# Performance work log

Hardware: AMD Instinct MI355X
Metric: run time of the kernel (lower is better)

The kernel has to match this reference:

```python
import jax, jax.numpy as jnp
import numpy as np

B, S, DM = 2, 2048, 1024
H, KH, HD = 16, 4, 64  # query heads, kv heads, head_dim
N_REP = H // KH


def rotate_half(u):
    d = u.shape[-1] // 2
    return jnp.concatenate([-u[..., d:], u[..., :d]], axis=-1)


def setup_inputs() -> dict:
    key = jax.random.key(0)
    ks = jax.random.split(key, 7)
    x = jax.random.normal(ks[0], (B, S, DM), dtype=jnp.float32)
    # RoPE tables (real rotary angles for realism)
    inv_freq = 1.0 / (10000.0 ** (jnp.arange(0, HD, 2, dtype=jnp.float32) / HD))
    t = jnp.arange(S, dtype=jnp.float32)
    freqs = jnp.outer(t, inv_freq)                      # [S, HD/2]
    emb = jnp.concatenate([freqs, freqs], axis=-1)      # [S, HD]
    cos, sin = jnp.cos(emb), jnp.sin(emb)
    sc = 0.02
    wq = jax.random.normal(ks[1], (DM, H * HD), dtype=jnp.float32) * sc
    wk = jax.random.normal(ks[2], (DM, KH * HD), dtype=jnp.float32) * sc
    wv = jax.random.normal(ks[3], (DM, KH * HD), dtype=jnp.float32) * sc
    wo = jax.random.normal(ks[4], (H * HD, DM), dtype=jnp.float32) * sc
    return {"x": x, "cos": cos, "sin": sin, "wq": wq, "wk": wk, "wv": wv, "wo": wo}


def reference(x, cos, sin, wq, wk, wv, wo):
    b, s, _ = x.shape
    # QKV projections (no bias)
    q = (x @ wq).reshape(b, s, H, HD)   # [b,s,H,HD]
    k = (x @ wk).reshape(b, s, KH, HD)  # [b,s,KH,HD]
    v = (x @ wv).reshape(b, s, KH, HD)
    # RoPE, broadcast cos/sin over the head axis
    c = cos[None, :s, None, :]
    sn = sin[None, :s, None, :]
    q = q * c + rotate_half(q) * sn
    k = k * c + rotate_half(k) * sn
    # GQA: repeat kv heads (repeat_interleave along head axis)
    k = jnp.repeat(k, N_REP, axis=2)  # [b,s,H,HD]
    v = jnp.repeat(v, N_REP, axis=2)
    # causal attention, full score matrix (non-flash path)
    scores = jnp.einsum("bqhd,bkhd->bhqk", q, k) / jnp.sqrt(jnp.float32(HD))
    causal = jnp.tril(jnp.ones((s, s), dtype=bool))
    scores = jnp.where(causal[None, None], scores, jnp.float32(-jnp.inf))
    attn = jax.nn.softmax(scores, axis=-1)
    out = jnp.einsum("bhqk,bkhd->bqhd", attn, v).reshape(b, s, H * HD)
    return out @ wo
```

## Files before the change

kernel.cpp:

```cpp
#include <hip/hip_runtime.h>
#include <hip/hip_bf16.h>

#define BATCH 2
#define SLEN  2048
#define DM    1024
#define NH    16
#define NKH   4
#define HD    64
#define NCH   4
#define PSTRIDE (BATCH * SLEN * NH * HD)
#define LSTRIDE (BATCH * SLEN * NH)

typedef __attribute__((ext_vector_type(8))) short short8;
typedef __attribute__((ext_vector_type(4))) float f32x4;

static __device__ __forceinline__ short f2bf(float x) {
    unsigned u = __float_as_uint(x);
    u += 0x7fffu + ((u >> 16) & 1u);
    return (short)(u >> 16);
}

static __device__ __forceinline__ void ldg_lds16(const short* g, short* l) {
    __builtin_amdgcn_global_load_lds(
        (const __attribute__((address_space(1))) unsigned int*)(const void*)g,
        (__attribute__((address_space(3))) unsigned int*)(void*)l,
        16, 0, 0);
}

#define QSCALE 0.1803368801f

__global__ void cvt_bf16(const float* __restrict__ X, short* __restrict__ Xb, int total8)
{
    const int i = blockIdx.x * blockDim.x + threadIdx.x;
    if (i >= total8) return;
    const float4 v0 = ((const float4*)X)[i * 2];
    const float4 v1 = ((const float4*)X)[i * 2 + 1];
    __align__(16) short o[8];
    o[0] = f2bf(v0.x); o[1] = f2bf(v0.y); o[2] = f2bf(v0.z); o[3] = f2bf(v0.w);
    o[4] = f2bf(v1.x); o[5] = f2bf(v1.y); o[6] = f2bf(v1.z); o[7] = f2bf(v1.w);
    ((int4*)Xb)[i] = *(const int4*)o;
}

__global__ __launch_bounds__(256) void wtrans_all(
    const float* __restrict__ wq, const float* __restrict__ wk,
    const float* __restrict__ wv, const float* __restrict__ wo,
    short* __restrict__ T)
{
    const int by = blockIdx.y;
    const float* W; int Nc, rowoff, ntile;
    if (by < 16)      { W = wq; Nc = 1024; rowoff = 0;    ntile = by; }
    else if (by < 20) { W = wk; Nc = 256;  rowoff = 1024; ntile = by - 16; }
    else if (by < 24) { W = wv; Nc = 256;  rowoff = 1280; ntile = by - 20; }
    else              { W = wo; Nc = 1024; rowoff = 1536; ntile = by - 24; }
    const int kt = blockIdx.x * 64;
    const int nt = ntile * 64;
    const int t  = threadIdx.x;
    __shared__ float tile[64][65];

#pragma unroll
    for (int i = 0; i < 4; ++i) {
        const int r = (t >> 4) + i * 16;
        const int c = (t & 15) * 4;
        const float4 v = *(const float4*)(W + (size_t)(kt + r) * Nc + nt + c);
        tile[r][c + 0] = v.x; tile[r][c + 1] = v.y;
        tile[r][c + 2] = v.z; tile[r][c + 3] = v.w;
    }
    __syncthreads();
#pragma unroll
    for (int i = 0; i < 2; ++i) {
        const int rr = (t >> 3) + i * 32;
        const int cc = (t & 7) * 8;
        __align__(16) short o[8];
#pragma unroll
        for (int j = 0; j < 8; ++j) o[j] = f2bf(tile[cc + j][rr]);
        *(int4*)(T + (size_t)(rowoff + nt + rr) * 1024 + kt + cc) = *(const int4*)o;
    }
}

template<int MODE>
__global__ __launch_bounds__(256) void gemm_abt(
    const short* __restrict__ A, const short* __restrict__ Bt,
    int M, int N, int K,
    float* __restrict__ Cf,
    short* __restrict__ Qb, short* __restrict__ Kb, short* __restrict__ Vb,
    const float* __restrict__ cosp, const float* __restrict__ sinp)
{
    const int t    = threadIdx.x;
    const int lane = t & 63;
    const int w    = t >> 6;
    const int l15  = lane & 15;
    const int l4   = lane >> 4;
    const int n0   = blockIdx.x * 128;
    const int m0   = blockIdx.y * 128;
    const int wm   = (w & 1) * 64;
    const int wn   = (w >> 1) * 64;

    __shared__ __align__(16) short As[128 * 32];
    __shared__ __align__(16) short Bs[128 * 32];

    f32x4 acc[4][4];
#pragma unroll
    for (int i = 0; i < 4; ++i)
#pragma unroll
        for (int j = 0; j < 4; ++j) acc[i][j] = (f32x4){0.f, 0.f, 0.f, 0.f};

    for (int kt = 0; kt < K; kt += 32) {
        __syncthreads();
#pragma unroll
        for (int i = 0; i < 2; ++i) {
            const int chunk = i * 256 + t;
            const int r = chunk >> 2;
            const int c = (chunk & 3) * 8;
            ldg_lds16(A  + (size_t)(m0 + r) * K + kt + c, &As[chunk * 8]);
            ldg_lds16(Bt + (size_t)(n0 + r) * K + kt + c, &Bs[chunk * 8]);
        }
        __syncthreads();

        short8 af[4], bf[4];
#pragma unroll
        for (int i = 0; i < 4; ++i)
            af[i] = *(const short8*)&As[(wm + i * 16 + l15) * 32 + l4 * 8];
#pragma unroll
        for (int j = 0; j < 4; ++j)
            bf[j] = *(const short8*)&Bs[(wn + j * 16 + l15) * 32 + l4 * 8];
#pragma unroll
        for (int i = 0; i < 4; ++i)
#pragma unroll
            for (int j = 0; j < 4; ++j)
                acc[i][j] = __builtin_amdgcn_mfma_f32_16x16x32_bf16(af[i], bf[j], acc[i][j], 0, 0, 0);
    }

    if (MODE == 1) {
#pragma unroll
        for (int i = 0; i < 4; ++i)
#pragma unroll
            for (int j = 0; j < 4; ++j)
#pragma unroll
                for (int r = 0; r < 4; ++r) {
                    const int m = m0 + wm + i * 16 + l4 * 4 + r;
                    const int n = n0 + wn + j * 16 + l15;
                    Cf[(size_t)m * N + n] = acc[i][j][r];
                }
        return;
    }

    const int colbase = n0 + wn;
    if (colbase < 1024) {
        const int h = colbase >> 6;
#pragma unroll
        for (int i = 0; i < 4; ++i)
#pragma unroll
            for (int r = 0; r < 4; ++r) {
                const int m = m0 + wm + i * 16 + l4 * 4 + r;
                const int b = m >> 11, s = m & (SLEN - 1);
                short* dst = Qb + (((size_t)(b * SLEN + s) * NH + h) << 6);
#pragma unroll
                for (int j = 0; j < 2; ++j) {
                    const int d = j * 16 + l15;
                    const float cv = cosp[s * HD + d];
                    const float sv = sinp[s * HD + d];
                    const float a0 = acc[i][j][r];
                    const float a1 = acc[i][j + 2][r];
                    dst[d]      = f2bf((a0 * cv - a1 * sv) * QSCALE);
                    dst[d + 32] = f2bf((a1 * cv + a0 * sv) * QSCALE);
                }
            }
    } else if (colbase < 1280) {
        const int kh = (colbase - 1024) >> 6;
#pragma unroll
        for (int i = 0; i < 4; ++i)
#pragma unroll
            for (int r = 0; r < 4; ++r) {
                const int m = m0 + wm + i * 16 + l4 * 4 + r;
                const int b = m >> 11, s = m & (SLEN - 1);
                short* dst = Kb + (((size_t)(b * SLEN + s) * NKH + kh) << 6);
#pragma unroll
                for (int j = 0; j < 2; ++j) {
                    const int d = j * 16 + l15;
                    const float cv = cosp[s * HD + d];
                    const float sv = sinp[s * HD + d];
                    const float a0 = acc[i][j][r];
                    const float a1 = acc[i][j + 2][r];
                    dst[d]      = f2bf(a0 * cv - a1 * sv);
                    dst[d + 32] = f2bf(a1 * cv + a0 * sv);
                }
            }
    } else {
        const int kh = (colbase - 1280) >> 6;
#pragma unroll
        for (int i = 0; i < 4; ++i)
#pragma unroll
            for (int r = 0; r < 4; ++r) {
                const int m = m0 + wm + i * 16 + l4 * 4 + r;
                const int b = m >> 11, s = m & (SLEN - 1);
                short* dst = Vb + (((size_t)(b * SLEN + s) * NKH + kh) << 6);
#pragma unroll
                for (int j = 0; j < 4; ++j)
                    dst[j * 16 + l15] = f2bf(acc[i][j][r]);
            }
    }
}

__global__ __launch_bounds__(256) void vtrans_b(
    const short* __restrict__ Vb, short* __restrict__ Vt)
{
    const int s0 = blockIdx.x * 64;
    const int kh = blockIdx.y;
    const int b  = blockIdx.z;
    const int t  = threadIdx.x;
    __shared__ short tile[64][72];

#pragma unroll
    for (int i = 0; i < 2; ++i) {
        const int chunk = i * 256 + t;
        const int r = chunk >> 3;
        const int c = (chunk & 7) * 8;
        *(int4*)&tile[r][c] =
            *(const int4*)(Vb + (((size_t)(b * SLEN + s0 + r) * NKH + kh) << 6) + c);
    }
    __syncthreads();
#pragma unroll
    for (int i = 0; i < 2; ++i) {
        const int chunk = i * 256 + t;
        const int d  = chunk >> 3;
        const int sc = (chunk & 7) * 8;
        __align__(16) short o[8];
#pragma unroll
        for (int j = 0; j < 8; ++j) {
            const int sp = sc + j;
            const int u  = ((sp & 3) << 4) | (sp >> 2);
            o[j] = tile[u][d];
        }
        *(int4*)(Vt + ((size_t)((b * NKH + kh) * HD + d)) * SLEN + s0 + sc) = *(const int4*)o;
    }
}

#define KVSTR 72

__global__ __launch_bounds__(256, 4) void flash_mfma(
    const short* __restrict__ Qb,
    const short* __restrict__ Kb,
    const short* __restrict__ Vt,
    short* __restrict__ O,
    float* __restrict__ Op,
    float* __restrict__ Lp)
{
    const int qs = 63 - blockIdx.x;
    const int kc = blockIdx.y & 3;
    if (kc * 16 > qs) return;
    const int kh = blockIdx.y >> 2;
    const int b  = blockIdx.z;
    const int t    = threadIdx.x;
    const int lane = t & 63;
    const int w    = t >> 6;
    const int h    = kh * 4 + w;
    const int l15  = lane & 15;
    const int l4   = lane >> 4;
    const int q0   = qs * 32;

    __shared__ __align__(16) short Ks[64 * KVSTR];
    __shared__ __align__(16) short Vs[64 * KVSTR];
    __shared__ __align__(16) short Ps[4][32 * KVSTR];

    short8 aq[2][2];
#pragma unroll
    for (int i = 0; i < 2; ++i)
#pragma unroll
        for (int ks = 0; ks < 2; ++ks)
            aq[i][ks] = *(const short8*)(
                Qb + ((size_t)((b * SLEN + q0 + i * 16 + l15) * NH + h)) * HD + ks * 32 + l4 * 8);

    f32x4 acc[2][4];
    f32x4 accl[2];
#pragma unroll
    for (int i = 0; i < 2; ++i) {
#pragma unroll
        for (int nt = 0; nt < 4; ++nt) acc[i][nt] = (f32x4){0.f, 0.f, 0.f, 0.f};
        accl[i] = (f32x4){0.f, 0.f, 0.f, 0.f};
    }

    const short8 ones8 = {0x3f80, 0x3f80, 0x3f80, 0x3f80, 0x3f80, 0x3f80, 0x3f80, 0x3f80};

    const int ntiles = (q0 >> 6) + 1;
    const int kt0  = kc * 8;
    const int kend = (kt0 + 8 < ntiles) ? kt0 + 8 : ntiles;

    for (int kt = kt0; kt < kend; ++kt) {
        const int k0 = kt * 64;
        __syncthreads();
#pragma unroll
        for (int i = 0; i < 2; ++i) {
            const int chunk = i * 256 + t;
            const int r = chunk >> 3;
            const int c = (chunk & 7) * 8;
            *(int4*)&Ks[r * KVSTR + c] =
                *(const int4*)(Kb + ((size_t)((b * SLEN + k0 + r) * NKH + kh)) * HD + c);
            *(int4*)&Vs[r * KVSTR + c] =
                *(const int4*)(Vt + ((size_t)((b * NKH + kh) * HD + r)) * SLEN + k0 + c);
        }
        __syncthreads();

        f32x4 sf[2][4];
#pragma unroll
        for (int i = 0; i < 2; ++i)
#pragma unroll
            for (int f = 0; f < 4; ++f) sf[i][f] = (f32x4){0.f, 0.f, 0.f, 0.f};
#pragma unroll
        for (int ks = 0; ks < 2; ++ks)
#pragma unroll
            for (int f = 0; f < 4; ++f) {
                const short8 bk = *(const short8*)&Ks[(f * 16 + l15) * KVSTR + ks * 32 + l4 * 8];
#pragma unroll
                for (int i = 0; i < 2; ++i)
                    sf[i][f] = __builtin_amdgcn_mfma_f32_16x16x32_bf16(aq[i][ks], bk, sf[i][f], 0, 0, 0);
            }

        if (kt == ntiles - 1) {
#pragma unroll
            for (int i = 0; i < 2; ++i)
#pragma unroll
                for (int f = 0; f < 4; ++f)
#pragma unroll
                    for (int r = 0; r < 4; ++r)
                        if (k0 + f * 16 + l15 > q0 + i * 16 + l4 * 4 + r)
                            sf[i][f][r] = -1e30f;
        }

#pragma unroll
        for (int i = 0; i < 2; ++i)
#pragma unroll
            for (int r = 0; r < 4; ++r) {
                __align__(8) short pk[4];
#pragma unroll
                for (int f = 0; f < 4; ++f) pk[f] = f2bf(exp2f(sf[i][f][r]));
                *(int2*)&Ps[w][(i * 16 + l4 * 4 + r) * KVSTR + 4 * l15] = *(const int2*)pk;
            }

#pragma unroll
        for (int ks = 0; ks < 2; ++ks) {
            short8 ap[2];
#pragma unroll
            for (int i = 0; i < 2; ++i)
                ap[i] = *(const short8*)&Ps[w][(i * 16 + l15) * KVSTR + ks * 32 + l4 * 8];
#pragma unroll
            for (int nt = 0; nt < 4; ++nt) {
                const short8 bv = *(const short8*)&Vs[(nt * 16 + l15) * KVSTR + ks * 32 + l4 * 8];
#pragma unroll
                for (int i = 0; i < 2; ++i)
                    acc[i][nt] = __builtin_amdgcn_mfma_f32_16x16x32_bf16(ap[i], bv, acc[i][nt], 0, 0, 0);
            }
#pragma unroll
            for (int i = 0; i < 2; ++i)
                accl[i] = __builtin_amdgcn_mfma_f32_16x16x32_bf16(ap[i], ones8, accl[i], 0, 0, 0);
        }
    }

    if (q0 < 512) {
#pragma unroll
        for (int i = 0; i < 2; ++i) {
            float rl[4];
#pragma unroll
            for (int r = 0; r < 4; ++r) rl[r] = 1.f / accl[i][r];
#pragma unroll
            for (int nt = 0; nt < 4; ++nt)
#pragma unroll
                for (int r = 0; r < 4; ++r) {
                    const int q = q0 + i * 16 + l4 * 4 + r;
                    O[((size_t)((b * SLEN + q) * NH + h)) * HD + nt * 16 + l15] =
                        f2bf(acc[i][nt][r] * rl[r]);
                }
        }
    } else {
        const size_t pbase = (size_t)kc * PSTRIDE;
#pragma unroll
        for (int i = 0; i < 2; ++i)
#pragma unroll
            for (int nt = 0; nt < 4; ++nt)
#pragma unroll
                for (int r = 0; r < 4; ++r) {
                    const int q = q0 + i * 16 + l4 * 4 + r;
                    Op[pbase + ((size_t)((b * SLEN + q) * NH + h)) * HD + nt * 16 + l15] =
                        acc[i][nt][r];
                }
        if (l15 == 0) {
#pragma unroll
            for (int i = 0; i < 2; ++i)
#pragma unroll
                for (int r = 0; r < 4; ++r) {
                    const int q = q0 + i * 16 + l4 * 4 + r;
                    Lp[(size_t)kc * LSTRIDE + (size_t)(b * SLEN + q) * NH + h] = accl[i][r];
                }
        }
    }
}

__global__ void combine_k(const float* __restrict__ Op, const float* __restrict__ Lp,
                          short* __restrict__ O)
{
    const int idx = blockIdx.x * 256 + threadIdx.x;
    const int dq = idx & 15;
    const int h  = (idx >> 4) & 15;
    const int rr = idx >> 8;
    const int b  = rr / 1536;
    const int s  = 512 + (rr - b * 1536);
    const int nact = (s >> 9) + 1;
    const size_t row = (size_t)(b * SLEN + s) * NH + h;

    float4 o = {0.f, 0.f, 0.f, 0.f};
    float l = 0.f;
    for (int kc = 0; kc < nact; ++kc) {
        const float4 p = *(const float4*)(Op + (size_t)kc * PSTRIDE + row * HD + dq * 4);
        o.x += p.x; o.y += p.y; o.z += p.z; o.w += p.w;
        l += Lp[(size_t)kc * LSTRIDE + row];
    }
    const float rl = 1.f / l;
    __align__(8) short pk[4];
    pk[0] = f2bf(o.x * rl); pk[1] = f2bf(o.y * rl);
    pk[2] = f2bf(o.z * rl); pk[3] = f2bf(o.w * rl);
    *(int2*)(O + row * HD + dq * 4) = *(const int2*)pk;
}

extern "C" void kernel_launch(void* const* d_in, const int* in_sizes, int n_in,
                              void* d_out, int out_size, void* d_ws, size_t ws_size,
                              hipStream_t stream) {
    const float* x    = (const float*)d_in[0];
    const float* cosp = (const float*)d_in[1];
    const float* sinp = (const float*)d_in[2];
    const float* wq   = (const float*)d_in[3];
    const float* wk   = (const float*)d_in[4];
    const float* wv   = (const float*)d_in[5];
    const float* wo   = (const float*)d_in[6];
    float* out = (float*)d_out;

    const int Mrows = BATCH * SLEN;

    short* xb = (short*)d_ws;
    short* Ob = xb;
    short* wT = xb + (size_t)Mrows * 1024;
    short* Qb = wT + (size_t)2560 * 1024;
    short* Kb = Qb + (size_t)Mrows * 1024;
    short* Vt = Kb + (size_t)Mrows * 256;
    short* Vb = Vt + (size_t)Mrows * 256;
    float* Op = (float*)(Vb + (size_t)Mrows * 256);
    float* Lp = Op + (size_t)NCH * PSTRIDE;

    cvt_bf16<<<(Mrows * DM / 8 + 255) / 256, 256, 0, stream>>>(x, xb, Mrows * DM / 8);

    wtrans_all<<<dim3(16, 40), 256, 0, stream>>>(wq, wk, wv, wo, wT);

    gemm_abt<0><<<dim3(1536 / 128, Mrows / 128), 256, 0, stream>>>(
        xb, wT, Mrows, 1536, DM, nullptr, Qb, Kb, Vb, cosp, sinp);

    vtrans_b<<<dim3(SLEN / 64, NKH, BATCH), 256, 0, stream>>>(Vb, Vt);

    flash_mfma<<<dim3(SLEN / 32, NKH * NCH, BATCH), 256, 0, stream>>>(
        Qb, Kb, Vt, Ob, Op, Lp);

    combine_k<<<(BATCH * 1536 * NH * 16) / 256, 256, 0, stream>>>(Op, Lp, Ob);

    gemm_abt<1><<<dim3(DM / 128, Mrows / 128), 256, 0, stream>>>(
        Ob, wT + (size_t)1536 * 1024, Mrows, DM, DM, out,
        nullptr, nullptr, nullptr, nullptr, nullptr);
}
```

Baseline: 204.2 us.

## Shrink GEMM M-tile with deeper K step; swizzle flash K/V LDS via direct loads

The GEMM tile changes from 128x128 with K-step 32 to 64x128 with K-step 64. This doubles the grid to improve CU occupancy on the projection GEMMs and halves the number of barriers per K. In the flash kernel, K and V tiles are now loaded with global_load_lds into unpadded, XOR-swizzled LDS instead of going through registers into padded rows. This aims to cut register staging and avoid bank conflicts. The trade-off is lower per-block data reuse in the GEMM, and the swizzled layout must exactly match the read indexing.

```diff
diff --git a/kernel.cpp b/kernel.cpp
--- a/kernel.cpp
+++ b/kernel.cpp
@@ -91,48 +91,57 @@
     const int l15  = lane & 15;
     const int l4   = lane >> 4;
     const int n0   = blockIdx.x * 128;
-    const int m0   = blockIdx.y * 128;
-    const int wm   = (w & 1) * 64;
+    const int m0   = blockIdx.y * 64;
+    const int wm   = (w & 1) * 32;
     const int wn   = (w >> 1) * 64;
 
-    __shared__ __align__(16) short As[128 * 32];
-    __shared__ __align__(16) short Bs[128 * 32];
-
-    f32x4 acc[4][4];
-#pragma unroll
-    for (int i = 0; i < 4; ++i)
+    __shared__ __align__(16) short As[64 * 64];
+    __shared__ __align__(16) short Bs[128 * 64];
+
+    f32x4 acc[2][4];
+#pragma unroll
+    for (int i = 0; i < 2; ++i)
 #pragma unroll
         for (int j = 0; j < 4; ++j) acc[i][j] = (f32x4){0.f, 0.f, 0.f, 0.f};
 
-    for (int kt = 0; kt < K; kt += 32) {
+    for (int kt = 0; kt < K; kt += 64) {
         __syncthreads();
 #pragma unroll
         for (int i = 0; i < 2; ++i) {
             const int chunk = i * 256 + t;
-            const int r = chunk >> 2;
-            const int c = (chunk & 3) * 8;
-            ldg_lds16(A  + (size_t)(m0 + r) * K + kt + c, &As[chunk * 8]);
+            const int r = chunk >> 3;
+            const int c = (chunk & 7) * 8;
+            ldg_lds16(A + (size_t)(m0 + r) * K + kt + c, &As[chunk * 8]);
+        }
+#pragma unroll
+        for (int i = 0; i < 4; ++i) {
+            const int chunk = i * 256 + t;
+            const int r = chunk >> 3;
+            const int c = (chunk & 7) * 8;
             ldg_lds16(Bt + (size_t)(n0 + r) * K + kt + c, &Bs[chunk * 8]);
         }
         __syncthreads();
 
-        short8 af[4], bf[4];
-#pragma unroll
-        for (int i = 0; i < 4; ++i)
-            af[i] = *(const short8*)&As[(wm + i * 16 + l15) * 32 + l4 * 8];
-#pragma unroll
-        for (int j = 0; j < 4; ++j)
-            bf[j] = *(const short8*)&Bs[(wn + j * 16 + l15) * 32 + l4 * 8];
-#pragma unroll
-        for (int i = 0; i < 4; ++i)
+#pragma unroll
+        for (int k2 = 0; k2 < 2; ++k2) {
+            short8 af[2], bf[4];
+#pragma unroll
+            for (int i = 0; i < 2; ++i)
+                af[i] = *(const short8*)&As[(wm + i * 16 + l15) * 64 + k2 * 32 + l4 * 8];
 #pragma unroll
             for (int j = 0; j < 4; ++j)
-                acc[i][j] = __builtin_amdgcn_mfma_f32_16x16x32_bf16(af[i], bf[j], acc[i][j], 0, 0, 0);
+                bf[j] = *(const short8*)&Bs[(wn + j * 16 + l15) * 64 + k2 * 32 + l4 * 8];
+#pragma unroll
+            for (int i = 0; i < 2; ++i)
+#pragma unroll
+                for (int j = 0; j < 4; ++j)
+                    acc[i][j] = __builtin_amdgcn_mfma_f32_16x16x32_bf16(af[i], bf[j], acc[i][j], 0, 0, 0);
+        }
     }
 
     if (MODE == 1) {
 #pragma unroll
-        for (int i = 0; i < 4; ++i)
+        for (int i = 0; i < 2; ++i)
 #pragma unroll
             for (int j = 0; j < 4; ++j)
 #pragma unroll
@@ -148,7 +157,7 @@
     if (colbase < 1024) {
         const int h = colbase >> 6;
 #pragma unroll
-        for (int i = 0; i < 4; ++i)
+        for (int i = 0; i < 2; ++i)
 #pragma unroll
             for (int r = 0; r < 4; ++r) {
                 const int m = m0 + wm + i * 16 + l4 * 4 + r;
@@ -168,7 +177,7 @@
     } else if (colbase < 1280) {
         const int kh = (colbase - 1024) >> 6;
 #pragma unroll
-        for (int i = 0; i < 4; ++i)
+        for (int i = 0; i < 2; ++i)
 #pragma unroll
             for (int r = 0; r < 4; ++r) {
                 const int m = m0 + wm + i * 16 + l4 * 4 + r;
@@ -188,7 +197,7 @@
     } else {
         const int kh = (colbase - 1280) >> 6;
 #pragma unroll
-        for (int i = 0; i < 4; ++i)
+        for (int i = 0; i < 2; ++i)
 #pragma unroll
             for (int r = 0; r < 4; ++r) {
                 const int m = m0 + wm + i * 16 + l4 * 4 + r;
@@ -235,7 +244,7 @@
     }
 }
 
-#define KVSTR 72
+#define PSTR 72
 
 __global__ __launch_bounds__(256, 4) void flash_mfma(
     const short* __restrict__ Qb,
@@ -257,10 +266,11 @@
     const int l15  = lane & 15;
     const int l4   = lane >> 4;
     const int q0   = qs * 32;
-
-    __shared__ __align__(16) short Ks[64 * KVSTR];
-    __shared__ __align__(16) short Vs[64 * KVSTR];
-    __shared__ __align__(16) short Ps[4][32 * KVSTR];
+    const int sw   = l15 & 7;
+
+    __shared__ __align__(16) short Ks[64 * 64];
+    __shared__ __align__(16) short Vs[64 * 64];
+    __shared__ __align__(16) short Ps[4][32 * PSTR];
 
     short8 aq[2][2];
 #pragma unroll
@@ -291,12 +301,13 @@
 #pragma unroll
         for (int i = 0; i < 2; ++i) {
             const int chunk = i * 256 + t;
-            const int r = chunk >> 3;
-            const int c = (chunk & 7) * 8;
-            *(int4*)&Ks[r * KVSTR + c] =
-                *(const int4*)(Kb + ((size_t)((b * SLEN + k0 + r) * NKH + kh)) * HD + c);
-            *(int4*)&Vs[r * KVSTR + c] =
-                *(const int4*)(Vt + ((size_t)((b * NKH + kh) * HD + r)) * SLEN + k0 + c);
+            const int r  = chunk >> 3;
+            const int c8 = chunk & 7;
+            const int cs = (c8 ^ (r & 7)) * 8;
+            ldg_lds16(Kb + ((size_t)((b * SLEN + k0 + r) * NKH + kh)) * HD + cs,
+                      &Ks[chunk * 8]);
+            ldg_lds16(Vt + ((size_t)((b * NKH + kh) * HD + r)) * SLEN + k0 + cs,
+                      &Vs[chunk * 8]);
         }
         __syncthreads();
 
@@ -309,7 +320,8 @@
         for (int ks = 0; ks < 2; ++ks)
 #pragma unroll
             for (int f = 0; f < 4; ++f) {
-                const short8 bk = *(const short8*)&Ks[(f * 16 + l15) * KVSTR + ks * 32 + l4 * 8];
+                const short8 bk = *(const short8*)
+                    &Ks[(f * 16 + l15) * 64 + ((ks * 4 + l4) ^ sw) * 8];
 #pragma unroll
                 for (int i = 0; i < 2; ++i)
                     sf[i][f] = __builtin_amdgcn_mfma_f32_16x16x32_bf16(aq[i][ks], bk, sf[i][f], 0, 0, 0);
@@ -333,7 +345,7 @@
                 __align__(8) short pk[4];
 #pragma unroll
                 for (int f = 0; f < 4; ++f) pk[f] = f2bf(exp2f(sf[i][f][r]));
-                *(int2*)&Ps[w][(i * 16 + l4 * 4 + r) * KVSTR + 4 * l15] = *(const int2*)pk;
+                *(int2*)&Ps[w][(i * 16 + l4 * 4 + r) * PSTR + 4 * l15] = *(const int2*)pk;
             }
 
 #pragma unroll
@@ -341,10 +353,11 @@
             short8 ap[2];
 #pragma unroll
             for (int i = 0; i < 2; ++i)
-                ap[i] = *(const short8*)&Ps[w][(i * 16 + l15) * KVSTR + ks * 32 + l4 * 8];
+                ap[i] = *(const short8*)&Ps[w][(i * 16 + l15) * PSTR + ks * 32 + l4 * 8];
 #pragma unroll
             for (int nt = 0; nt < 4; ++nt) {
-                const short8 bv = *(const short8*)&Vs[(nt * 16 + l15) * KVSTR + ks * 32 + l4 * 8];
+                const short8 bv = *(const short8*)
+                    &Vs[(nt * 16 + l15) * 64 + ((ks * 4 + l4) ^ sw) * 8];
 #pragma unroll
                 for (int i = 0; i < 2; ++i)
                     acc[i][nt] = __builtin_amdgcn_mfma_f32_16x16x32_bf16(ap[i], bv, acc[i][nt], 0, 0, 0);
@@ -448,7 +461,7 @@
 
     wtrans_all<<<dim3(16, 40), 256, 0, stream>>>(wq, wk, wv, wo, wT);
 
-    gemm_abt<0><<<dim3(1536 / 128, Mrows / 128), 256, 0, stream>>>(
+    gemm_abt<0><<<dim3(1536 / 128, Mrows / 64), 256, 0, stream>>>(
         xb, wT, Mrows, 1536, DM, nullptr, Qb, Kb, Vb, cosp, sinp);
 
     vtrans_b<<<dim3(SLEN / 64, NKH, BATCH), 256, 0, stream>>>(Vb, Vt);
@@ -458,7 +471,7 @@
 
     combine_k<<<(BATCH * 1536 * NH * 16) / 256, 256, 0, stream>>>(Op, Lp, Ob);
 
-    gemm_abt<1><<<dim3(DM / 128, Mrows / 128), 256, 0, stream>>>(
+    gemm_abt<1><<<dim3(DM / 128, Mrows / 64), 256, 0, stream>>>(
         Ob, wT + (size_t)1536 * 1024, Mrows, DM, DM, out,
         nullptr, nullptr, nullptr, nullptr, nullptr);
 }
```

Result: faster. 191.2 us (-6.4%).
